# Kernel tuning notes

Hardware: AMD Instinct MI355X
Metric: run time of the kernel (lower is better)

Reference implementation:

```python
import jax, jax.numpy as jnp
import numpy as np

N_NODES = 100000
N_EDGES = 1600000
NUM_GRAPHS = 128
IN_F = 32
K = 3  # TAGConv default number of hops


def setup_inputs() -> dict:
    key = jax.random.key(0)
    ks = jax.random.split(key, 12)
    x = jax.random.normal(ks[0], (N_NODES, IN_F), dtype=jnp.float32)
    edge_index = jax.random.randint(ks[1], (2, N_EDGES), 0, N_NODES, dtype=jnp.int32)
    batch = jnp.sort(jax.random.randint(ks[2], (N_NODES,), 0, NUM_GRAPHS, dtype=jnp.int32))
    edge_weight = jax.random.uniform(ks[3], (N_EDGES,), dtype=jnp.float32)
    # TAGConv params: K+1 weight matrices per layer (bias shared per layer)
    s1 = 1.0 / np.sqrt(IN_F)
    s2 = 1.0 / np.sqrt(8)
    s3 = 1.0 / np.sqrt(32)
    W1 = jax.random.uniform(ks[4], (K + 1, IN_F, 8), jnp.float32, -s1, s1)
    b1 = jax.random.uniform(ks[5], (8,), jnp.float32, -s1, s1)
    W2 = jax.random.uniform(ks[6], (K + 1, 8, 16), jnp.float32, -s2, s2)
    b2 = jax.random.uniform(ks[7], (16,), jnp.float32, -s2, s2)
    Wfc = jax.random.uniform(ks[8], (32, 2), jnp.float32, -s3, s3)
    bfc = jax.random.uniform(ks[9], (2,), jnp.float32, -s3, s3)
    return {"x": x, "edge_index": edge_index, "batch": batch, "edge_weight": edge_weight,
            "W1": W1, "b1": b1, "W2": W2, "b2": b2, "Wfc": Wfc, "bfc": bfc}


def reference(x, edge_index, batch, edge_weight, W1, b1, W2, b2, Wfc, bfc):
    src, dst = edge_index[0], edge_index[1]
    n = x.shape[0]
    # gcn_norm without self-loops (TAGConv default): D^-1/2 A D^-1/2
    deg = jax.ops.segment_sum(edge_weight, dst, num_segments=n)
    dinv = jnp.where(deg > 0, jax.lax.rsqrt(jnp.maximum(deg, 1e-30)), 0.0)
    norm = dinv[src] * edge_weight * dinv[dst]

    def tag_conv(h, W, b):
        out = h @ W[0]
        for k in range(1, W.shape[0]):
            # sparse propagate: gather at src, scale, scatter-add at dst
            h = jax.ops.segment_sum(h[src] * norm[:, None], dst, num_segments=n)
            out = out + h @ W[k]
        return out + b

    h = jax.nn.relu(tag_conv(x, W1, b1))
    h = jax.nn.relu(tag_conv(h, W2, b2))
    # global max pool + global mean pool over graphs in the batch
    mx = jax.ops.segment_max(h, batch, num_segments=NUM_GRAPHS)
    cnt = jax.ops.segment_sum(jnp.ones((n,), h.dtype), batch, num_segments=NUM_GRAPHS)
    mean = jax.ops.segment_sum(h, batch, num_segments=NUM_GRAPHS) / jnp.maximum(cnt, 1.0)[:, None]
    return jnp.concatenate([mx, mean], axis=1) @ Wfc + bfc
```

## Files before the change

kernel.cpp:

```cpp
#include <hip/hip_runtime.h>

constexpr int NN = 100000;
constexpr int NE = 1600000;
constexpr int NG = 128;

constexpr int SCAN_T = 256;
constexpr int SCAN_B = (NN + SCAN_T - 1) / SCAN_T;

struct __align__(8) Ent { int s; float nw; };


__global__ void k_rank(const int4* __restrict__ dst4, int* __restrict__ cnt,
                       ushort4* __restrict__ rank4, int ne4) {
    int i = blockIdx.x * blockDim.x + threadIdx.x;
    if (i >= ne4) return;
    int4 d = dst4[i];
    ushort4 r;
    r.x = (ushort)atomicAdd(&cnt[d.x], 1);
    r.y = (ushort)atomicAdd(&cnt[d.y], 1);
    r.z = (ushort)atomicAdd(&cnt[d.z], 1);
    r.w = (ushort)atomicAdd(&cnt[d.w], 1);
    rank4[i] = r;
}

__global__ void k_scan1b(const int* __restrict__ cnt, int* __restrict__ bsum,
                         const int* __restrict__ batch, int* __restrict__ gstart, int nn) {
    __shared__ int s[SCAN_T];
    int b = blockIdx.x;
    if (b < SCAN_B) {
        int i = b * SCAN_T + threadIdx.x;
        s[threadIdx.x] = (i < nn) ? ((cnt[i] + 1) & ~1) : 0;
        __syncthreads();
        for (int off = SCAN_T / 2; off > 0; off >>= 1) {
            if (threadIdx.x < off) s[threadIdx.x] += s[threadIdx.x + off];
            __syncthreads();
        }
        if (threadIdx.x == 0) bsum[b] = s[0];
    } else {
        int i = (b - SCAN_B) * SCAN_T + threadIdx.x;
        if (i >= nn) return;
        int bb = batch[i];
        int prev = (i == 0) ? -1 : batch[i - 1];
        for (int g = prev + 1; g <= bb; ++g) gstart[g] = i;
        if (i == nn - 1) {
            for (int g = bb + 1; g <= NG; ++g) gstart[g] = nn;
        }
    }
}

__global__ void k_scan2(int* __restrict__ bsum, int nb) {
    __shared__ int s[512];
    int t = threadIdx.x;
    s[t] = (t < nb) ? bsum[t] : 0;
    __syncthreads();
    for (int off = 1; off < 512; off <<= 1) {
        int v = (t >= off) ? s[t - off] : 0;
        __syncthreads();
        s[t] += v;
        __syncthreads();
    }
    if (t < nb) bsum[t] = (t > 0) ? s[t - 1] : 0;
}

__global__ void k_scan3(const int* __restrict__ cnt, const int* __restrict__ bsum,
                        int* __restrict__ row_ptr, Ent* __restrict__ csr, int nn) {
    __shared__ int s[SCAN_T];
    int t = threadIdx.x;
    int i = blockIdx.x * SCAN_T + t;
    int c0 = (i < nn) ? cnt[i] : 0;
    int v = (c0 + 1) & ~1;
    s[t] = v;
    __syncthreads();
    for (int off = 1; off < SCAN_T; off <<= 1) {
        int u = (t >= off) ? s[t - off] : 0;
        __syncthreads();
        s[t] += u;
        __syncthreads();
    }
    int incl = s[t];
    int base = bsum[blockIdx.x];
    if (i < nn) {
        int rp = base + incl - v;
        row_ptr[i] = rp;
        if (i == nn - 1) row_ptr[nn] = base + incl;
        if (c0 & 1) {
            Ent z; z.s = 0; z.nw = 0.f;
            csr[rp + c0] = z;
        }
    }
}

__global__ void k_scatter2(const int4* __restrict__ src4, const int4* __restrict__ dst4,
                           const float4* __restrict__ w4, const int* __restrict__ row_ptr,
                           const ushort4* __restrict__ rank4, Ent* __restrict__ csr, int ne4) {
    int i = blockIdx.x * blockDim.x + threadIdx.x;
    if (i >= ne4) return;
    int4 s = src4[i]; int4 d = dst4[i]; float4 w = w4[i]; ushort4 r = rank4[i];
    Ent e0; e0.s = s.x; e0.nw = w.x; csr[row_ptr[d.x] + r.x] = e0;
    Ent e1; e1.s = s.y; e1.nw = w.y; csr[row_ptr[d.y] + r.y] = e1;
    Ent e2; e2.s = s.z; e2.nw = w.z; csr[row_ptr[d.z] + r.z] = e2;
    Ent e3; e3.s = s.w; e3.nw = w.w; csr[row_ptr[d.w] + r.w] = e3;
}

__global__ void k_degi(const int* __restrict__ row_ptr, const float4* __restrict__ csr4,
                       float* __restrict__ dinv, int nn) {
    int tid = blockIdx.x * blockDim.x + threadIdx.x;
    int n = tid >> 3, lane = tid & 7;
    if (n >= nn) return;
    int beg = row_ptr[n] >> 1, end = row_ptr[n + 1] >> 1;
    float s = 0.f;
    for (int p = beg + lane; p < end; p += 8) {
        float4 a = csr4[p];
        s += a.y + a.w;
    }
    s += __shfl_xor(s, 1, 64);
    s += __shfl_xor(s, 2, 64);
    s += __shfl_xor(s, 4, 64);
    if (lane == 0) dinv[n] = s > 0.f ? rsqrtf(fmaxf(s, 1e-30f)) : 0.f;
}

template <int FIN, int FOUT>
__global__ void k_mm4(const float* __restrict__ h, const float* __restrict__ W,
                      const float* __restrict__ dinv, float* __restrict__ t, int nn) {
    __shared__ float sW[4 * FIN * FOUT];
    for (int i = threadIdx.x; i < 4 * FIN * FOUT; i += blockDim.x) sW[i] = W[i];
    __syncthreads();
    int n = blockIdx.x * blockDim.x + threadIdx.x;
    if (n >= nn) return;
    float hr[FIN];
    const float4* hp = reinterpret_cast<const float4*>(h + (size_t)n * FIN);
#pragma unroll
    for (int f = 0; f < FIN / 4; ++f) {
        float4 v = hp[f];
        hr[4 * f + 0] = v.x; hr[4 * f + 1] = v.y;
        hr[4 * f + 2] = v.z; hr[4 * f + 3] = v.w;
    }
    float dv = dinv[n];
#pragma unroll
    for (int k = 0; k < 4; ++k) {
        float acc[FOUT];
#pragma unroll
        for (int j = 0; j < FOUT; ++j) acc[j] = 0.f;
#pragma unroll
        for (int i = 0; i < FIN; ++i) {
            float hv = hr[i];
            const float* wrow = &sW[(k * FIN + i) * FOUT];
#pragma unroll
            for (int j = 0; j < FOUT; ++j) acc[j] = fmaf(hv, wrow[j], acc[j]);
        }
        if (k == 3) {
#pragma unroll
            for (int j = 0; j < FOUT; ++j) acc[j] *= dv;
        }
        float4* op = reinterpret_cast<float4*>(t + ((size_t)k * nn + n) * FOUT);
#pragma unroll
        for (int j4 = 0; j4 < FOUT / 4; ++j4)
            op[j4] = make_float4(acc[4 * j4], acc[4 * j4 + 1], acc[4 * j4 + 2], acc[4 * j4 + 3]);
    }
}

template <int F, bool FINAL>
__global__ void k_pull(const int* __restrict__ row_ptr, const float4* __restrict__ csr4,
                       const float* __restrict__ dinv,
                       const float* __restrict__ hin, const float* __restrict__ add,
                       const float* __restrict__ b, float* __restrict__ hout, int nn) {
    int g = blockIdx.x * (blockDim.x / F) + threadIdx.x / F;
    int lane = threadIdx.x & (F - 1);
    if (g >= nn) return;
    int p = row_ptr[g] >> 1, end = row_ptr[g + 1] >> 1;
    float acc0 = 0.f, acc1 = 0.f, acc2 = 0.f, acc3 = 0.f;
    for (; p + 2 <= end; p += 2) {
        float4 a = csr4[p], c = csr4[p + 1];
        acc0 = fmaf(hin[(size_t)__float_as_int(a.x) * F + lane], a.y, acc0);
        acc1 = fmaf(hin[(size_t)__float_as_int(a.z) * F + lane], a.w, acc1);
        acc2 = fmaf(hin[(size_t)__float_as_int(c.x) * F + lane], c.y, acc2);
        acc3 = fmaf(hin[(size_t)__float_as_int(c.z) * F + lane], c.w, acc3);
    }
    if (p < end) {
        float4 a = csr4[p];
        acc0 = fmaf(hin[(size_t)__float_as_int(a.x) * F + lane], a.y, acc0);
        acc1 = fmaf(hin[(size_t)__float_as_int(a.z) * F + lane], a.w, acc1);
    }
    float acc = (acc0 + acc1) + (acc2 + acc3);
    float dv = dinv[g];
    float r;
    if (FINAL) r = fmaxf(dv * acc + add[(size_t)g * F + lane] + b[lane], 0.f);
    else       r = dv * (dv * acc + add[(size_t)g * F + lane]);
    hout[(size_t)g * F + lane] = r;
}


__global__ void k_pool2(const float* __restrict__ h, const int* __restrict__ start,
                        const float* __restrict__ Wfc, const float* __restrict__ bfc,
                        float* __restrict__ out) {
    int g = blockIdx.x;
    int beg = start[g], end = start[g + 1];
    int tid = threadIdx.x;
    int feat = tid & 15, grp = tid >> 4;
    float mx = 0.f, sm = 0.f;
    for (int n = beg + grp; n < end; n += 16) {
        float v = h[(size_t)n * 16 + feat];
        mx = fmaxf(mx, v);
        sm += v;
    }
    mx = fmaxf(mx, __shfl_xor(mx, 16, 64));
    sm += __shfl_xor(sm, 16, 64);
    mx = fmaxf(mx, __shfl_xor(mx, 32, 64));
    sm += __shfl_xor(sm, 32, 64);
    __shared__ float smx[4][16], ssm[4][16];
    int wave = tid >> 6;
    int lane = tid & 63;
    if (lane < 16) { smx[wave][feat] = mx; ssm[wave][feat] = sm; }
    __syncthreads();
    if (tid < 16) {
        float m = fmaxf(fmaxf(smx[0][tid], smx[1][tid]), fmaxf(smx[2][tid], smx[3][tid]));
        float s = ssm[0][tid] + ssm[1][tid] + ssm[2][tid] + ssm[3][tid];
        smx[0][tid] = m;
        ssm[0][tid] = (end > beg) ? s / (float)(end - beg) : 0.f;
    }
    __syncthreads();
    if (tid < 2) {
        float acc = bfc[tid];
#pragma unroll
        for (int i = 0; i < 16; ++i) acc += smx[0][i] * Wfc[i * 2 + tid];
#pragma unroll
        for (int i = 0; i < 16; ++i) acc += ssm[0][i] * Wfc[(16 + i) * 2 + tid];
        out[g * 2 + tid] = acc;
    }
}


extern "C" void kernel_launch(void* const* d_in, const int* in_sizes, int n_in,
                              void* d_out, int out_size, void* d_ws, size_t ws_size,
                              hipStream_t stream) {
    const float* x    = (const float*)d_in[0];
    const int*   eidx = (const int*)d_in[1];
    const int*   srcp = eidx;
    const int*   dstp = eidx + NE;
    const int*   batch= (const int*)d_in[2];
    const float* ew   = (const float*)d_in[3];
    const float* W1   = (const float*)d_in[4];
    const float* b1   = (const float*)d_in[5];
    const float* W2   = (const float*)d_in[6];
    const float* b2   = (const float*)d_in[7];
    const float* Wfc  = (const float*)d_in[8];
    const float* bfc  = (const float*)d_in[9];
    float* out = (float*)d_out;

    constexpr size_t NN8  = (size_t)NN * 8;
    constexpr size_t NN16 = (size_t)NN * 16;

    float*  dinv    = (float*)d_ws;
    int*    cnt     = (int*)(dinv + NN);
    int*    row_ptr = cnt + NN;
    ushort* rank    = (ushort*)(row_ptr + NN + 4);
    Ent*    csr     = (Ent*)((int*)(void*)rank + NE / 2);
    float*  uni     = (float*)(csr + NE + NN);
    float*  h1      = uni + 5 * NN16;
    int*    gstart  = (int*)(h1 + NN8);
    int*    bsum    = gstart + NG + 4;

    float* T  = uni;
    float* P  = uni + 2 * NN16;
    float* P2 = P + NN8;
    float* U    = uni;
    float* q    = uni + 4 * NN16;
    float* q2   = U + 3 * NN16;
    float* out2 = U + 2 * NN16;

    const float4* csr4 = (const float4*)csr;

    const int BLK = 256;
    const int NE4 = NE / 4;
    const int gE4 = (NE4 + BLK - 1) / BLK;
    const int gN  = (NN + BLK - 1) / BLK;
    const int gP8  = (NN + (BLK / 8) - 1) / (BLK / 8);
    const int gP16 = (NN + (BLK / 16) - 1) / (BLK / 16);
    const int gN8  = (NN * 8 + BLK - 1) / BLK;

    hipMemsetAsync(cnt, 0, (size_t)NN * sizeof(int), stream);
    k_rank<<<gE4, BLK, 0, stream>>>((const int4*)dstp, cnt, (ushort4*)rank, NE4);
    k_scan1b<<<SCAN_B + gN, SCAN_T, 0, stream>>>(cnt, bsum, batch, gstart, NN);
    k_scan2<<<1, 512, 0, stream>>>(bsum, SCAN_B);
    k_scan3<<<SCAN_B, SCAN_T, 0, stream>>>(cnt, bsum, row_ptr, csr, NN);
    k_scatter2<<<gE4, BLK, 0, stream>>>((const int4*)srcp, (const int4*)dstp,
                                        (const float4*)ew, row_ptr, (const ushort4*)rank,
                                        csr, NE4);
    k_degi<<<gN8, BLK, 0, stream>>>(row_ptr, csr4, dinv, NN);

    k_mm4<32, 8><<<gN, BLK, 0, stream>>>(x, W1, dinv, T, NN);
    k_pull<8, false><<<gP8, BLK, 0, stream>>>(row_ptr, csr4, dinv, T + 3 * NN8, T + 2 * NN8, nullptr, P, NN);
    k_pull<8, false><<<gP8, BLK, 0, stream>>>(row_ptr, csr4, dinv, P, T + 1 * NN8, nullptr, P2, NN);
    k_pull<8, true ><<<gP8, BLK, 0, stream>>>(row_ptr, csr4, dinv, P2, T, b1, h1, NN);

    k_mm4<8, 16><<<gN, BLK, 0, stream>>>(h1, W2, dinv, U, NN);
    k_pull<16, false><<<gP16, BLK, 0, stream>>>(row_ptr, csr4, dinv, U + 3 * NN16, U + 2 * NN16, nullptr, q, NN);
    k_pull<16, false><<<gP16, BLK, 0, stream>>>(row_ptr, csr4, dinv, q, U + 1 * NN16, nullptr, q2, NN);
    k_pull<16, true ><<<gP16, BLK, 0, stream>>>(row_ptr, csr4, dinv, q2, U, b2, out2, NN);

    k_pool2<<<NG, 256, 0, stream>>>(out2, gstart, Wfc, bfc, out);
}
```

Measured before the change: 305.3 us.

## Fuse layer-2 matmul into pull kernels and use decoupled-lookback single-pass scan

Replaces the three-kernel scan (block sums, scan of sums, final scan) with a single-pass decoupled lookback scan that also fills the graph start table. It removes the separate layer-2 k_mm4 kernel: the last layer-1 pull now computes h1 and the W2[3] projection in registers via shuffles, and each layer-2 pull recomputes h1 @ W2[k] on the fly instead of reading a precomputed buffer. This cuts kernel launches and the large U write/read traffic, in exchange for redundant small matmuls per pull and a serial spin-wait lookback chain across blocks in the scan.

```diff
diff --git a/kernel.cpp b/kernel.cpp
--- a/kernel.cpp
+++ b/kernel.cpp
@@ -23,69 +23,55 @@
     rank4[i] = r;
 }
 
-__global__ void k_scan1b(const int* __restrict__ cnt, int* __restrict__ bsum,
+__global__ void k_scanDL(const int* __restrict__ cnt, unsigned long long* __restrict__ state,
+                         int* __restrict__ row_ptr, Ent* __restrict__ csr,
                          const int* __restrict__ batch, int* __restrict__ gstart, int nn) {
     __shared__ int s[SCAN_T];
-    int b = blockIdx.x;
-    if (b < SCAN_B) {
-        int i = b * SCAN_T + threadIdx.x;
-        s[threadIdx.x] = (i < nn) ? ((cnt[i] + 1) & ~1) : 0;
+    __shared__ int sbase;
+    int b = blockIdx.x, t = threadIdx.x;
+    int i = b * SCAN_T + t;
+    int c0 = (i < nn) ? cnt[i] : 0;
+    int v = (c0 + 1) & ~1;
+    s[t] = v;
+    __syncthreads();
+    for (int off = 1; off < SCAN_T; off <<= 1) {
+        int u = (t >= off) ? s[t - off] : 0;
         __syncthreads();
-        for (int off = SCAN_T / 2; off > 0; off >>= 1) {
-            if (threadIdx.x < off) s[threadIdx.x] += s[threadIdx.x + off];
-            __syncthreads();
-        }
-        if (threadIdx.x == 0) bsum[b] = s[0];
-    } else {
-        int i = (b - SCAN_B) * SCAN_T + threadIdx.x;
-        if (i >= nn) return;
+        s[t] += u;
+        __syncthreads();
+    }
+    if (t == 0) {
+        int agg = s[SCAN_T - 1];
+        __hip_atomic_store(&state[b], (1ull << 62) | (unsigned)agg,
+                           __ATOMIC_RELEASE, __HIP_MEMORY_SCOPE_AGENT);
+        int excl = 0;
+        for (int j = b - 1; j >= 0; --j) {
+            unsigned long long st;
+            do {
+                st = __hip_atomic_load(&state[j], __ATOMIC_ACQUIRE, __HIP_MEMORY_SCOPE_AGENT);
+            } while ((st >> 62) == 0);
+            excl += (int)(st & 0xffffffffull);
+            if ((st >> 62) == 2) break;
+        }
+        __hip_atomic_store(&state[b], (2ull << 62) | (unsigned)(excl + agg),
+                           __ATOMIC_RELEASE, __HIP_MEMORY_SCOPE_AGENT);
+        sbase = excl;
+    }
+    __syncthreads();
+    int base = sbase;
+    if (i < nn) {
+        int rp = base + s[t] - v;
+        row_ptr[i] = rp;
+        if (i == nn - 1) row_ptr[nn] = base + s[t];
+        if (c0 & 1) {
+            Ent z; z.s = 0; z.nw = 0.f;
+            csr[rp + c0] = z;
+        }
         int bb = batch[i];
         int prev = (i == 0) ? -1 : batch[i - 1];
         for (int g = prev + 1; g <= bb; ++g) gstart[g] = i;
         if (i == nn - 1) {
             for (int g = bb + 1; g <= NG; ++g) gstart[g] = nn;
-        }
-    }
-}
-
-__global__ void k_scan2(int* __restrict__ bsum, int nb) {
-    __shared__ int s[512];
-    int t = threadIdx.x;
-    s[t] = (t < nb) ? bsum[t] : 0;
-    __syncthreads();
-    for (int off = 1; off < 512; off <<= 1) {
-        int v = (t >= off) ? s[t - off] : 0;
-        __syncthreads();
-        s[t] += v;
-        __syncthreads();
-    }
-    if (t < nb) bsum[t] = (t > 0) ? s[t - 1] : 0;
-}
-
-__global__ void k_scan3(const int* __restrict__ cnt, const int* __restrict__ bsum,
-                        int* __restrict__ row_ptr, Ent* __restrict__ csr, int nn) {
-    __shared__ int s[SCAN_T];
-    int t = threadIdx.x;
-    int i = blockIdx.x * SCAN_T + t;
-    int c0 = (i < nn) ? cnt[i] : 0;
-    int v = (c0 + 1) & ~1;
-    s[t] = v;
-    __syncthreads();
-    for (int off = 1; off < SCAN_T; off <<= 1) {
-        int u = (t >= off) ? s[t - off] : 0;
-        __syncthreads();
-        s[t] += u;
-        __syncthreads();
-    }
-    int incl = s[t];
-    int base = bsum[blockIdx.x];
-    if (i < nn) {
-        int rp = base + incl - v;
-        row_ptr[i] = rp;
-        if (i == nn - 1) row_ptr[nn] = base + incl;
-        if (c0 & 1) {
-            Ent z; z.s = 0; z.nw = 0.f;
-            csr[rp + c0] = z;
         }
     }
 }
@@ -119,18 +105,17 @@
     if (lane == 0) dinv[n] = s > 0.f ? rsqrtf(fmaxf(s, 1e-30f)) : 0.f;
 }
 
-template <int FIN, int FOUT>
 __global__ void k_mm4(const float* __restrict__ h, const float* __restrict__ W,
                       const float* __restrict__ dinv, float* __restrict__ t, int nn) {
-    __shared__ float sW[4 * FIN * FOUT];
-    for (int i = threadIdx.x; i < 4 * FIN * FOUT; i += blockDim.x) sW[i] = W[i];
+    __shared__ float sW[4 * 32 * 8];
+    for (int i = threadIdx.x; i < 4 * 32 * 8; i += blockDim.x) sW[i] = W[i];
     __syncthreads();
     int n = blockIdx.x * blockDim.x + threadIdx.x;
     if (n >= nn) return;
-    float hr[FIN];
-    const float4* hp = reinterpret_cast<const float4*>(h + (size_t)n * FIN);
-#pragma unroll
-    for (int f = 0; f < FIN / 4; ++f) {
+    float hr[32];
+    const float4* hp = reinterpret_cast<const float4*>(h + (size_t)n * 32);
+#pragma unroll
+    for (int f = 0; f < 8; ++f) {
         float4 v = hp[f];
         hr[4 * f + 0] = v.x; hr[4 * f + 1] = v.y;
         hr[4 * f + 2] = v.z; hr[4 * f + 3] = v.w;
@@ -138,32 +123,31 @@
     float dv = dinv[n];
 #pragma unroll
     for (int k = 0; k < 4; ++k) {
-        float acc[FOUT];
-#pragma unroll
-        for (int j = 0; j < FOUT; ++j) acc[j] = 0.f;
-#pragma unroll
-        for (int i = 0; i < FIN; ++i) {
+        float acc[8];
+#pragma unroll
+        for (int j = 0; j < 8; ++j) acc[j] = 0.f;
+#pragma unroll
+        for (int i = 0; i < 32; ++i) {
             float hv = hr[i];
-            const float* wrow = &sW[(k * FIN + i) * FOUT];
-#pragma unroll
-            for (int j = 0; j < FOUT; ++j) acc[j] = fmaf(hv, wrow[j], acc[j]);
+            const float* wrow = &sW[(k * 32 + i) * 8];
+#pragma unroll
+            for (int j = 0; j < 8; ++j) acc[j] = fmaf(hv, wrow[j], acc[j]);
         }
         if (k == 3) {
 #pragma unroll
-            for (int j = 0; j < FOUT; ++j) acc[j] *= dv;
-        }
-        float4* op = reinterpret_cast<float4*>(t + ((size_t)k * nn + n) * FOUT);
-#pragma unroll
-        for (int j4 = 0; j4 < FOUT / 4; ++j4)
-            op[j4] = make_float4(acc[4 * j4], acc[4 * j4 + 1], acc[4 * j4 + 2], acc[4 * j4 + 3]);
-    }
-}
-
-template <int F, bool FINAL>
-__global__ void k_pull(const int* __restrict__ row_ptr, const float4* __restrict__ csr4,
-                       const float* __restrict__ dinv,
-                       const float* __restrict__ hin, const float* __restrict__ add,
-                       const float* __restrict__ b, float* __restrict__ hout, int nn) {
+            for (int j = 0; j < 8; ++j) acc[j] *= dv;
+        }
+        float4* op = reinterpret_cast<float4*>(t + ((size_t)k * nn + n) * 8);
+        op[0] = make_float4(acc[0], acc[1], acc[2], acc[3]);
+        op[1] = make_float4(acc[4], acc[5], acc[6], acc[7]);
+    }
+}
+
+__global__ void k_pull8(const int* __restrict__ row_ptr, const float4* __restrict__ csr4,
+                        const float* __restrict__ dinv,
+                        const float* __restrict__ hin, const float* __restrict__ add,
+                        float* __restrict__ hout, int nn) {
+    constexpr int F = 8;
     int g = blockIdx.x * (blockDim.x / F) + threadIdx.x / F;
     int lane = threadIdx.x & (F - 1);
     if (g >= nn) return;
@@ -183,9 +167,92 @@
     }
     float acc = (acc0 + acc1) + (acc2 + acc3);
     float dv = dinv[g];
+    hout[(size_t)g * F + lane] = dv * (dv * acc + add[(size_t)g * F + lane]);
+}
+
+__global__ void k_pull8_final(const int* __restrict__ row_ptr, const float4* __restrict__ csr4,
+                              const float* __restrict__ dinv,
+                              const float* __restrict__ hin, const float* __restrict__ add,
+                              const float* __restrict__ b1, const float* __restrict__ W23,
+                              float* __restrict__ h1, float* __restrict__ U3, int nn) {
+    __shared__ float sW[8 * 16];
+    if (threadIdx.x < 128) sW[threadIdx.x] = W23[threadIdx.x];
+    __syncthreads();
+    constexpr int F = 8;
+    int g = blockIdx.x * (blockDim.x / F) + threadIdx.x / F;
+    int lane = threadIdx.x & (F - 1);
+    if (g >= nn) return;
+    int p = row_ptr[g] >> 1, end = row_ptr[g + 1] >> 1;
+    float acc0 = 0.f, acc1 = 0.f, acc2 = 0.f, acc3 = 0.f;
+    for (; p + 2 <= end; p += 2) {
+        float4 a = csr4[p], c = csr4[p + 1];
+        acc0 = fmaf(hin[(size_t)__float_as_int(a.x) * F + lane], a.y, acc0);
+        acc1 = fmaf(hin[(size_t)__float_as_int(a.z) * F + lane], a.w, acc1);
+        acc2 = fmaf(hin[(size_t)__float_as_int(c.x) * F + lane], c.y, acc2);
+        acc3 = fmaf(hin[(size_t)__float_as_int(c.z) * F + lane], c.w, acc3);
+    }
+    if (p < end) {
+        float4 a = csr4[p];
+        acc0 = fmaf(hin[(size_t)__float_as_int(a.x) * F + lane], a.y, acc0);
+        acc1 = fmaf(hin[(size_t)__float_as_int(a.z) * F + lane], a.w, acc1);
+    }
+    float acc = (acc0 + acc1) + (acc2 + acc3);
+    float dv = dinv[g];
+    float r = fmaxf(dv * acc + add[(size_t)g * F + lane] + b1[lane], 0.f);
+    h1[(size_t)g * F + lane] = r;
+    float u0 = 0.f, u1 = 0.f;
+#pragma unroll
+    for (int i = 0; i < 8; ++i) {
+        float hv = __shfl(r, i, 8);
+        u0 = fmaf(hv, sW[i * 16 + lane], u0);
+        u1 = fmaf(hv, sW[i * 16 + lane + 8], u1);
+    }
+    U3[(size_t)g * 16 + lane] = dv * u0;
+    U3[(size_t)g * 16 + lane + 8] = dv * u1;
+}
+
+template <bool FINAL>
+__global__ void k_pullW(const int* __restrict__ row_ptr, const float4* __restrict__ csr4,
+                        const float* __restrict__ dinv,
+                        const float* __restrict__ hin, const float* __restrict__ h1,
+                        const float* __restrict__ W2k, const float* __restrict__ b2,
+                        float* __restrict__ hout, int nn) {
+    __shared__ float sW[8 * 16];
+    if (threadIdx.x < 128) sW[threadIdx.x] = W2k[threadIdx.x];
+    __syncthreads();
+    constexpr int F = 16;
+    int g = blockIdx.x * (blockDim.x / F) + threadIdx.x / F;
+    int lane = threadIdx.x & (F - 1);
+    if (g >= nn) return;
+    int p = row_ptr[g] >> 1, end = row_ptr[g + 1] >> 1;
+    float acc0 = 0.f, acc1 = 0.f, acc2 = 0.f, acc3 = 0.f;
+    for (; p + 2 <= end; p += 2) {
+        float4 a = csr4[p], c = csr4[p + 1];
+        acc0 = fmaf(hin[(size_t)__float_as_int(a.x) * F + lane], a.y, acc0);
+        acc1 = fmaf(hin[(size_t)__float_as_int(a.z) * F + lane], a.w, acc1);
+        acc2 = fmaf(hin[(size_t)__float_as_int(c.x) * F + lane], c.y, acc2);
+        acc3 = fmaf(hin[(size_t)__float_as_int(c.z) * F + lane], c.w, acc3);
+    }
+    if (p < end) {
+        float4 a = csr4[p];
+        acc0 = fmaf(hin[(size_t)__float_as_int(a.x) * F + lane], a.y, acc0);
+        acc1 = fmaf(hin[(size_t)__float_as_int(a.z) * F + lane], a.w, acc1);
+    }
+    float acc = (acc0 + acc1) + (acc2 + acc3);
+    const float4* h1p = reinterpret_cast<const float4*>(h1 + (size_t)g * 8);
+    float4 ha = h1p[0], hb = h1p[1];
+    float add = ha.x * sW[0 * 16 + lane];
+    add = fmaf(ha.y, sW[1 * 16 + lane], add);
+    add = fmaf(ha.z, sW[2 * 16 + lane], add);
+    add = fmaf(ha.w, sW[3 * 16 + lane], add);
+    add = fmaf(hb.x, sW[4 * 16 + lane], add);
+    add = fmaf(hb.y, sW[5 * 16 + lane], add);
+    add = fmaf(hb.z, sW[6 * 16 + lane], add);
+    add = fmaf(hb.w, sW[7 * 16 + lane], add);
+    float dv = dinv[g];
     float r;
-    if (FINAL) r = fmaxf(dv * acc + add[(size_t)g * F + lane] + b[lane], 0.f);
-    else       r = dv * (dv * acc + add[(size_t)g * F + lane]);
+    if (FINAL) r = fmaxf(dv * acc + add + b2[lane], 0.f);
+    else       r = dv * (dv * acc + add);
     hout[(size_t)g * F + lane] = r;
 }
 
@@ -252,21 +319,21 @@
 
     float*  dinv    = (float*)d_ws;
     int*    cnt     = (int*)(dinv + NN);
-    int*    row_ptr = cnt + NN;
+    unsigned long long* state = (unsigned long long*)(cnt + NN);
+    int*    row_ptr = (int*)(state + SCAN_B + 1);
     ushort* rank    = (ushort*)(row_ptr + NN + 4);
     Ent*    csr     = (Ent*)((int*)(void*)rank + NE / 2);
     float*  uni     = (float*)(csr + NE + NN);
-    float*  h1      = uni + 5 * NN16;
+    float*  h1      = uni + 4 * NN16;
     int*    gstart  = (int*)(h1 + NN8);
-    int*    bsum    = gstart + NG + 4;
 
     float* T  = uni;
     float* P  = uni + 2 * NN16;
     float* P2 = P + NN8;
-    float* U    = uni;
-    float* q    = uni + 4 * NN16;
-    float* q2   = U + 3 * NN16;
-    float* out2 = U + 2 * NN16;
+    float* U3   = uni + 3 * NN16;
+    float* q    = uni + 0 * NN16;
+    float* q2   = uni + 1 * NN16;
+    float* out2 = uni + 2 * NN16;
 
     const float4* csr4 = (const float4*)csr;
 
@@ -278,25 +345,23 @@
     const int gP16 = (NN + (BLK / 16) - 1) / (BLK / 16);
     const int gN8  = (NN * 8 + BLK - 1) / BLK;
 
-    hipMemsetAsync(cnt, 0, (size_t)NN * sizeof(int), stream);
+    hipMemsetAsync(cnt, 0, (size_t)NN * sizeof(int) + (SCAN_B + 1) * sizeof(unsigned long long), stream);
     k_rank<<<gE4, BLK, 0, stream>>>((const int4*)dstp, cnt, (ushort4*)rank, NE4);
-    k_scan1b<<<SCAN_B + gN, SCAN_T, 0, stream>>>(cnt, bsum, batch, gstart, NN);
-    k_scan2<<<1, 512, 0, stream>>>(bsum, SCAN_B);
-    k_scan3<<<SCAN_B, SCAN_T, 0, stream>>>(cnt, bsum, row_ptr, csr, NN);
+    k_scanDL<<<SCAN_B, SCAN_T, 0, stream>>>(cnt, state, row_ptr, csr, batch, gstart, NN);
     k_scatter2<<<gE4, BLK, 0, stream>>>((const int4*)srcp, (const int4*)dstp,
                                         (const float4*)ew, row_ptr, (const ushort4*)rank,
                                         csr, NE4);
     k_degi<<<gN8, BLK, 0, stream>>>(row_ptr, csr4, dinv, NN);
 
-    k_mm4<32, 8><<<gN, BLK, 0, stream>>>(x, W1, dinv, T, NN);
-    k_pull<8, false><<<gP8, BLK, 0, stream>>>(row_ptr, csr4, dinv, T + 3 * NN8, T + 2 * NN8, nullptr, P, NN);
-    k_pull<8, false><<<gP8, BLK, 0, stream>>>(row_ptr, csr4, dinv, P, T + 1 * NN8, nullptr, P2, NN);
-    k_pull<8, true ><<<gP8, BLK, 0, stream>>>(row_ptr, csr4, dinv, P2, T, b1, h1, NN);
-
-    k_mm4<8, 16><<<gN, BLK, 0, stream>>>(h1, W2, dinv, U, NN);
-    k_pull<16, false><<<gP16, BLK, 0, stream>>>(row_ptr, csr4, dinv, U + 3 * NN16, U + 2 * NN16, nullptr, q, NN);
-    k_pull<16, false><<<gP16, BLK, 0, stream>>>(row_ptr, csr4, dinv, q, U + 1 * NN16, nullptr, q2, NN);
-    k_pull<16, true ><<<gP16, BLK, 0, stream>>>(row_ptr, csr4, dinv, q2, U, b2, out2, NN);
+    k_mm4<<<gN, BLK, 0, stream>>>(x, W1, dinv, T, NN);
+    k_pull8<<<gP8, BLK, 0, stream>>>(row_ptr, csr4, dinv, T + 3 * NN8, T + 2 * NN8, P, NN);
+    k_pull8<<<gP8, BLK, 0, stream>>>(row_ptr, csr4, dinv, P, T + 1 * NN8, P2, NN);
+    k_pull8_final<<<gP8, BLK, 0, stream>>>(row_ptr, csr4, dinv, P2, T, b1,
+                                           W2 + 3 * 128, h1, U3, NN);
+
+    k_pullW<false><<<gP16, BLK, 0, stream>>>(row_ptr, csr4, dinv, U3, h1, W2 + 2 * 128, nullptr, q, NN);
+    k_pullW<false><<<gP16, BLK, 0, stream>>>(row_ptr, csr4, dinv, q,  h1, W2 + 1 * 128, nullptr, q2, NN);
+    k_pullW<true ><<<gP16, BLK, 0, stream>>>(row_ptr, csr4, dinv, q2, h1, W2 + 0 * 128, b2, out2, NN);
 
     k_pool2<<<NG, 256, 0, stream>>>(out2, gstart, Wfc, bfc, out);
 }
```

After: 404.2 us. 1.32x slower.
